# Kernel tuning notes

Hardware: AMD Instinct MI355X
Metric: run time of the kernel (lower is better)

The kernel has to match this reference:

```python
import jax, jax.numpy as jnp
import numpy as np

N_HEAD = 8
HEAD_DIM = 32  # 256 / 8
MASK_VALUE = -10000.0

def setup_inputs() -> dict:
    key = jax.random.key(0)
    k1, k2, k3 = jax.random.split(key, 3)
    B, S, D = 8, 2048, 256
    x = jax.random.normal(k1, (B, S, D), dtype=jnp.float32)
    # kaiming_normal fan_in-based std ~ sqrt(2/fan_in)
    w_qkv = jax.random.normal(k2, (3 * D, D), dtype=jnp.float32) * np.sqrt(2.0 / D)
    b_qkv = jnp.zeros((3 * D,), dtype=jnp.float32)
    w_out = jax.random.normal(k3, (D, D), dtype=jnp.float32) * np.sqrt(2.0 / D)
    b_out = jnp.zeros((D,), dtype=jnp.float32)
    return {"x": x, "w_qkv": w_qkv, "b_qkv": b_qkv, "w_out": w_out, "b_out": b_out}

def reference(x, w_qkv, b_qkv, w_out, b_out):
    B, S, D = x.shape
    qkv = x @ w_qkv.T + b_qkv                      # [B,S,3D]
    q, k, v = jnp.split(qkv, 3, axis=-1)           # each [B,S,D]
    def split_heads(t):
        return t.reshape(B, S, N_HEAD, HEAD_DIM).transpose(0, 2, 1, 3)  # [B,H,S,hd]
    q, k, v = split_heads(q), split_heads(k), split_heads(v)
    scores = jnp.einsum('bhqd,bhkd->bhqk', q, k) / jnp.sqrt(jnp.float32(HEAD_DIM))
    causal = jnp.tril(jnp.ones((S, S), dtype=bool))
    scores = jnp.where(causal[None, None], scores, jnp.float32(MASK_VALUE))
    attn = jax.nn.softmax(scores, axis=-1)          # dropout p=0 (eval)
    out = jnp.einsum('bhqk,bhkd->bhqd', attn, v)    # [B,H,S,hd]
    out = out.transpose(0, 2, 1, 3).reshape(B, S, D)  # merge heads
    out = out @ w_out.T + b_out
    return (out, attn)
```

## Files before the change

### kernel.cpp

```cpp
#include <hip/hip_runtime.h>
#include <cmath>

#define NB 8
#define NS 2048
#define ND 256
#define NH 8
#define HD 32
#define NM (NB*NS)
#define QS_LOG2 (0.17677669529663689f * 1.4426950408889634f)
#define OUT_ATTN ((size_t)NM * ND)

typedef __attribute__((ext_vector_type(8))) short bf16x8;
typedef __attribute__((ext_vector_type(4))) float f32x4;

__device__ __forceinline__ ushort f2b(float f) {
  union { float f; uint32_t u; } v; v.f = f;
  const uint32_t r = (v.u + 0x7FFFu + ((v.u >> 16) & 1u)) >> 16;
  return (ushort)r;
}
__device__ __forceinline__ float b2f(ushort u) {
  union { uint32_t u; float f; } v; v.u = ((uint32_t)u) << 16;
  return v.f;
}

__global__ __launch_bounds__(256) void prep_kernel(
    const float* __restrict__ x, const float* __restrict__ wq,
    const float* __restrict__ wo,
    ushort* __restrict__ xh, ushort* __restrict__ xl,
    ushort* __restrict__ wqh, ushort* __restrict__ wql,
    ushort* __restrict__ woh) {
  const int g = blockIdx.x * 256 + threadIdx.x;
  if (g < 1048576) {
    const float4 v = ((const float4*)x)[g];
    ushort4 h, l;
    h.x = f2b(v.x); l.x = f2b(v.x - b2f(h.x));
    h.y = f2b(v.y); l.y = f2b(v.y - b2f(h.y));
    h.z = f2b(v.z); l.z = f2b(v.z - b2f(h.z));
    h.w = f2b(v.w); l.w = f2b(v.w - b2f(h.w));
    ((ushort4*)xh)[g] = h; ((ushort4*)xl)[g] = l;
  } else if (g < 1048576 + 49152) {
    const int t = g - 1048576;
    const float4 v = ((const float4*)wq)[t];
    ushort4 h, l;
    h.x = f2b(v.x); l.x = f2b(v.x - b2f(h.x));
    h.y = f2b(v.y); l.y = f2b(v.y - b2f(h.y));
    h.z = f2b(v.z); l.z = f2b(v.z - b2f(h.z));
    h.w = f2b(v.w); l.w = f2b(v.w - b2f(h.w));
    ((ushort4*)wqh)[t] = h; ((ushort4*)wql)[t] = l;
  } else if (g < 1048576 + 49152 + 16384) {
    const int t = g - (1048576 + 49152);
    const float4 v = ((const float4*)wo)[t];
    ushort4 h;
    h.x = f2b(v.x); h.y = f2b(v.y); h.z = f2b(v.z); h.w = f2b(v.w);
    ((ushort4*)woh)[t] = h;
  }
}

__global__ __launch_bounds__(256) void qkv_kernel(
    const ushort* __restrict__ xh, const ushort* __restrict__ xl,
    const ushort* __restrict__ wqh, const ushort* __restrict__ wql,
    const float* __restrict__ bias,
    ushort* __restrict__ Qb, ushort* __restrict__ Kb, ushort* __restrict__ Vt) {
  __shared__ ushort Bh[128][40];
  __shared__ ushort Bl[128][40];
  const int m0 = blockIdx.x * 64;
  const int n0 = blockIdx.y * 128;
  const int tid  = threadIdx.x;
  const int w = tid >> 6, lane = tid & 63;
  const int a = lane & 15, qd = lane >> 4;
  const int srow = tid & 127, sop = tid >> 7;
  const f32x4 zero4 = {0.f, 0.f, 0.f, 0.f};
  f32x4 acc[8] = {zero4, zero4, zero4, zero4, zero4, zero4, zero4, zero4};

  const size_t arow = (size_t)(m0 + w*16 + a) * ND;
  const ushort* __restrict__ bsrc = (sop ? wql : wqh) + (size_t)(n0 + srow) * ND;

  for (int ks = 0; ks < 8; ++ks) {
    const int kofs = ks * 32;
    const bf16x8 t0 = *(const bf16x8*)&bsrc[kofs + 0];
    const bf16x8 t1 = *(const bf16x8*)&bsrc[kofs + 8];
    const bf16x8 t2 = *(const bf16x8*)&bsrc[kofs + 16];
    const bf16x8 t3 = *(const bf16x8*)&bsrc[kofs + 24];
    const bf16x8 ah = *(const bf16x8*)&xh[arow + kofs + qd*8];
    const bf16x8 al = *(const bf16x8*)&xl[arow + kofs + qd*8];
    __syncthreads();
    ushort (* __restrict__ Bs)[40] = sop ? Bl : Bh;
    *(bf16x8*)&Bs[srow][0]  = t0;
    *(bf16x8*)&Bs[srow][8]  = t1;
    *(bf16x8*)&Bs[srow][16] = t2;
    *(bf16x8*)&Bs[srow][24] = t3;
    __syncthreads();
#pragma unroll
    for (int nt = 0; nt < 8; ++nt) {
      const bf16x8 bhf = *(const bf16x8*)&Bh[nt*16 + a][qd*8];
      const bf16x8 blf = *(const bf16x8*)&Bl[nt*16 + a][qd*8];
      acc[nt] = __builtin_amdgcn_mfma_f32_16x16x32_bf16(al, bhf, acc[nt], 0, 0, 0);
      acc[nt] = __builtin_amdgcn_mfma_f32_16x16x32_bf16(ah, blf, acc[nt], 0, 0, 0);
      acc[nt] = __builtin_amdgcn_mfma_f32_16x16x32_bf16(ah, bhf, acc[nt], 0, 0, 0);
    }
  }

  const int mbase = m0 + w*16 + qd*4;
  const int bb = mbase >> 11, ss = mbase & 2047;
#pragma unroll
  for (int nt = 0; nt < 8; ++nt) {
    const int n = n0 + nt*16 + a;
    const int which = n >> 8;
    const int h = (n >> 5) & 7, e0 = n & 31;
    const float bz = bias[n];
    if (which < 2) {
      const float scl = (which == 0) ? QS_LOG2 : 1.0f;
      ushort* const dst = ((which == 0) ? Qb : Kb) + (size_t)(bb*NH + h) * NS * HD;
#pragma unroll
      for (int r = 0; r < 4; ++r)
        dst[(size_t)(ss + r) * HD + e0] = f2b((acc[nt][r] + bz) * scl);
    } else {
      ushort4 o;
      o.x = f2b(acc[nt][0] + bz);
      o.y = f2b(acc[nt][1] + bz);
      o.z = f2b(acc[nt][2] + bz);
      o.w = f2b(acc[nt][3] + bz);
      *(ushort4*)&Vt[((size_t)(bb*NH + h)*HD + e0) * NS + ss] = o;
    }
  }
}

__global__ __launch_bounds__(256) void attn_kernel(
    const ushort* __restrict__ Qb, const ushort* __restrict__ Kb,
    const ushort* __restrict__ Vt, float* __restrict__ attn,
    ushort* __restrict__ Om) {
  __shared__ float Ps[2][64][68];
  const int bh = blockIdx.x;
  const int by = blockIdx.y;
  const int qt = (by & 1) ? (by >> 1) : (NS/64 - 1 - (by >> 1));
  const int q0 = qt * 64;
  const int lane = threadIdx.x & 63;
  const int w    = threadIdx.x >> 6;
  const int a    = lane & 15;
  const int qd   = lane >> 4;
  const ushort* __restrict__ Qh = Qb + (size_t)bh * NS * HD;
  const ushort* __restrict__ Kh = Kb + (size_t)bh * NS * HD;
  const ushort* __restrict__ Vh = Vt + (size_t)bh * HD * NS;

  const f32x4 zero4 = {0.f, 0.f, 0.f, 0.f};
  const bf16x8 qf = *(const bf16x8*)&Qh[(size_t)(q0 + w*16 + a) * HD + qd*8];
  float* const attnRow = attn + ((size_t)bh * NS + q0) * NS;

  bf16x8 kf[4], kn[4], vf[4], vp[4];
#pragma unroll
  for (int jt = 0; jt < 4; ++jt)
    kf[jt] = *(const bf16x8*)&Kh[(size_t)(jt*16 + a) * HD + qd*8];

  float l_l[4] = {0.f, 0.f, 0.f, 0.f};
  int zt = qt + 1;
  for (int kt = 0; kt <= qt; ++kt) {
    const bool diag = (kt == qt);
    const int lim = diag ? w : 3;
    if (kt < qt) {
      const int k0n = (kt + 1) * 64;
#pragma unroll
      for (int jt = 0; jt < 4; ++jt)
        kn[jt] = *(const bf16x8*)&Kh[(size_t)(k0n + jt*16 + a) * HD + qd*8];
    }
    if (zt < NS / 64) {
      const int z0 = zt * 64;
#pragma unroll
      for (int i = 0; i < 4; ++i)
        __builtin_nontemporal_store(zero4,
            (f32x4*)&attnRow[(size_t)(w*16 + i*4 + qd) * NS + z0 + a*4]);
      ++zt;
    }
    __builtin_amdgcn_s_setprio(1);
#pragma unroll
    for (int jt = 0; jt < 4; ++jt) {
      if (jt > lim) continue;
      const f32x4 s = __builtin_amdgcn_mfma_f32_16x16x32_bf16(qf, kf[jt], zero4, 0, 0, 0);
      if (diag && jt == w) {
#pragma unroll
        for (int r = 0; r < 4; ++r)
          l_l[r] += (a > qd*4 + r) ? 0.f : exp2f(s[r]);
      } else {
#pragma unroll
        for (int r = 0; r < 4; ++r)
          l_l[r] += exp2f(s[r]);
      }
    }
    __builtin_amdgcn_s_setprio(0);
#pragma unroll
    for (int jt = 0; jt < 4; ++jt) kf[jt] = kn[jt];
  }

#pragma unroll
  for (int jt = 0; jt < 4; ++jt)
    kf[jt] = *(const bf16x8*)&Kh[(size_t)(jt*16 + a) * HD + qd*8];
  vf[0] = *(const bf16x8*)&Vh[(size_t)(a)      * NS + qd*8];
  vf[1] = *(const bf16x8*)&Vh[(size_t)(16 + a) * NS + qd*8];
  vf[2] = *(const bf16x8*)&Vh[(size_t)(a)      * NS + 32 + qd*8];
  vf[3] = *(const bf16x8*)&Vh[(size_t)(16 + a) * NS + 32 + qd*8];

  for (; zt < NS / 64; ++zt) {
    const int z0 = zt * 64;
#pragma unroll
    for (int i = 0; i < 4; ++i)
      __builtin_nontemporal_store(zero4,
          (f32x4*)&attnRow[(size_t)(w*16 + i*4 + qd) * NS + z0 + a*4]);
  }

  float mc[4];
#pragma unroll
  for (int r = 0; r < 4; ++r) {
    float c = l_l[r];
#pragma unroll
    for (int off = 1; off < 16; off <<= 1) c += __shfl_xor(c, off);
    mc[r] = log2f(c);
  }

  f32x4 oc0 = zero4, oc1 = zero4;
  int buf = 0;

  for (int kt = 0; kt <= qt; ++kt) {
    const int k0 = kt * 64;
    const bool diag = (kt == qt);
    const int lim = diag ? w : 3;

    if (kt < qt) {
      const int k0n = k0 + 64;
#pragma unroll
      for (int jt = 0; jt < 4; ++jt)
        kn[jt] = *(const bf16x8*)&Kh[(size_t)(k0n + jt*16 + a) * HD + qd*8];
    }
    if (kt > 0) {
      vf[0] = *(const bf16x8*)&Vh[(size_t)(a)      * NS + k0 + qd*8];
      vf[1] = *(const bf16x8*)&Vh[(size_t)(16 + a) * NS + k0 + qd*8];
      vf[2] = *(const bf16x8*)&Vh[(size_t)(a)      * NS + k0 + 32 + qd*8];
      vf[3] = *(const bf16x8*)&Vh[(size_t)(16 + a) * NS + k0 + 32 + qd*8];
    }

    __builtin_amdgcn_s_setprio(1);
#pragma unroll
    for (int jt = 0; jt < 4; ++jt) {
      if (jt > lim) {
#pragma unroll
        for (int r = 0; r < 4; ++r)
          Ps[buf][w*16 + qd*4 + r][jt*16 + a] = 0.f;
        continue;
      }
      const f32x4 s = __builtin_amdgcn_mfma_f32_16x16x32_bf16(qf, kf[jt], zero4, 0, 0, 0);
      if (diag && jt == w) {
#pragma unroll
        for (int r = 0; r < 4; ++r)
          Ps[buf][w*16 + qd*4 + r][jt*16 + a] =
              (a > qd*4 + r) ? 0.f : exp2f(s[r] - mc[r]);
      } else {
#pragma unroll
        for (int r = 0; r < 4; ++r)
          Ps[buf][w*16 + qd*4 + r][jt*16 + a] = exp2f(s[r] - mc[r]);
      }
    }
    __builtin_amdgcn_s_setprio(0);

#pragma unroll
    for (int i = 0; i < 4; ++i) {
      const int row16 = i*4 + qd;
      const f32x4 pv = *(const f32x4*)&Ps[buf][w*16 + row16][a*4];
      __builtin_nontemporal_store(pv,
          (f32x4*)&attnRow[(size_t)(w*16 + row16) * NS + k0 + a*4]);
    }

    if (kt > 0) {
      __builtin_amdgcn_s_setprio(1);
#pragma unroll
      for (int half = 0; half < 2; ++half) {
        const float4 p0 = *(const float4*)&Ps[buf ^ 1][w*16 + a][half*32 + qd*8];
        const float4 p1 = *(const float4*)&Ps[buf ^ 1][w*16 + a][half*32 + qd*8 + 4];
        bf16x8 pa;
        pa[0] = (short)f2b(p0.x); pa[1] = (short)f2b(p0.y);
        pa[2] = (short)f2b(p0.z); pa[3] = (short)f2b(p0.w);
        pa[4] = (short)f2b(p1.x); pa[5] = (short)f2b(p1.y);
        pa[6] = (short)f2b(p1.z); pa[7] = (short)f2b(p1.w);
        oc0 = __builtin_amdgcn_mfma_f32_16x16x32_bf16(pa, half ? vp[2] : vp[0], oc0, 0, 0, 0);
        oc1 = __builtin_amdgcn_mfma_f32_16x16x32_bf16(pa, half ? vp[3] : vp[1], oc1, 0, 0, 0);
      }
      __builtin_amdgcn_s_setprio(0);
    }

#pragma unroll
    for (int jt = 0; jt < 4; ++jt) { kf[jt] = kn[jt]; vp[jt] = vf[jt]; }
    buf ^= 1;
  }

  {
    __builtin_amdgcn_s_setprio(1);
#pragma unroll
    for (int half = 0; half < 2; ++half) {
      const float4 p0 = *(const float4*)&Ps[buf ^ 1][w*16 + a][half*32 + qd*8];
      const float4 p1 = *(const float4*)&Ps[buf ^ 1][w*16 + a][half*32 + qd*8 + 4];
      bf16x8 pa;
      pa[0] = (short)f2b(p0.x); pa[1] = (short)f2b(p0.y);
      pa[2] = (short)f2b(p0.z); pa[3] = (short)f2b(p0.w);
      pa[4] = (short)f2b(p1.x); pa[5] = (short)f2b(p1.y);
      pa[6] = (short)f2b(p1.z); pa[7] = (short)f2b(p1.w);
      oc0 = __builtin_amdgcn_mfma_f32_16x16x32_bf16(pa, half ? vp[2] : vp[0], oc0, 0, 0, 0);
      oc1 = __builtin_amdgcn_mfma_f32_16x16x32_bf16(pa, half ? vp[3] : vp[1], oc1, 0, 0, 0);
    }
    __builtin_amdgcn_s_setprio(0);
  }

  const int bb = bh >> 3, hh = bh & 7;
#pragma unroll
  for (int r = 0; r < 4; ++r) {
    const size_t om = (size_t)(bb * NS + q0 + w*16 + qd*4 + r) * ND + hh*32;
    Om[om + a]      = f2b(oc0[r]);
    Om[om + 16 + a] = f2b(oc1[r]);
  }
}

__global__ __launch_bounds__(256) void proj_kernel(
    const ushort* __restrict__ Om, const ushort* __restrict__ woh,
    const float* __restrict__ bias, float* __restrict__ out) {
  const int m0 = blockIdx.x * 64;
  const int nb = blockIdx.y * 64;
  const int w = threadIdx.x >> 6, lane = threadIdx.x & 63;
  const int a = lane & 15, qd = lane >> 4;
  const f32x4 zero4 = {0.f, 0.f, 0.f, 0.f};
  f32x4 acc[4] = {zero4, zero4, zero4, zero4};
  const size_t arow = (size_t)(m0 + w*16 + a) * ND;
#pragma unroll
  for (int ks = 0; ks < 8; ++ks) {
    const int kofs = ks * 32 + qd * 8;
    const bf16x8 af = *(const bf16x8*)&Om[arow + kofs];
#pragma unroll
    for (int nt = 0; nt < 4; ++nt) {
      const bf16x8 bfg = *(const bf16x8*)&woh[(size_t)(nb + nt*16 + a) * ND + kofs];
      acc[nt] = __builtin_amdgcn_mfma_f32_16x16x32_bf16(af, bfg, acc[nt], 0, 0, 0);
    }
  }
#pragma unroll
  for (int nt = 0; nt < 4; ++nt) {
    const int n = nb + nt*16 + a;
    const float bz = bias[n];
#pragma unroll
    for (int r = 0; r < 4; ++r)
      out[(size_t)(m0 + w*16 + qd*4 + r) * ND + n] = acc[nt][r] + bz;
  }
}

extern "C" void kernel_launch(void* const* d_in, const int* in_sizes, int n_in,
                              void* d_out, int out_size, void* d_ws, size_t ws_size,
                              hipStream_t stream) {
  const float* x     = (const float*)d_in[0];
  const float* w_qkv = (const float*)d_in[1];
  const float* b_qkv = (const float*)d_in[2];
  const float* w_out = (const float*)d_in[3];
  const float* b_out = (const float*)d_in[4];
  float* out  = (float*)d_out;
  float* attn = out + OUT_ATTN;

  ushort* u = (ushort*)d_ws;
  const size_t SZH = (size_t)NB * NH * NS * HD;
  ushort* Qb  = u;  u += SZH;
  ushort* Kb  = u;  u += SZH;
  ushort* Vt  = u;  u += SZH;
  ushort* Om  = u;  u += SZH;
  ushort* xh  = u;  u += SZH;
  ushort* xl  = u;  u += SZH;
  ushort* wqh = u;  u += (size_t)768 * ND;
  ushort* wql = u;  u += (size_t)768 * ND;
  ushort* woh = u;  u += (size_t)ND * ND;

  prep_kernel<<<4352, 256, 0, stream>>>(x, w_qkv, w_out, xh, xl, wqh, wql, woh);
  qkv_kernel<<<dim3(NM / 64, 768 / 128), 256, 0, stream>>>(xh, xl, wqh, wql, b_qkv, Qb, Kb, Vt);
  attn_kernel<<<dim3(NB * NH, NS / 64), 256, 0, stream>>>(Qb, Kb, Vt, attn, Om);
  proj_kernel<<<dim3(NM / 64, ND / 64), 256, 0, stream>>>(Om, woh, b_out, out);
}
```

Measured before the change: 307.9 us.

## Pair high and low causal query tiles per block for load balance

Each attention block now handles two query tiles, one from the top and one from the bottom of the causal triangle (j and NS/64-1-j), so every block does roughly the same amount of work. The grid is halved. Zero-fill stores for one tile are interleaved with the row-sum pass of the other, which is meant to hide store traffic behind compute. In exchange there are half as many blocks to fill the GPU, and register pressure rises from holding two Q fragments and two sets of softmax statistics.

```diff
diff --git a/kernel.cpp b/kernel.cpp
--- a/kernel.cpp
+++ b/kernel.cpp
@@ -131,9 +131,10 @@
     ushort* __restrict__ Om) {
   __shared__ float Ps[2][64][68];
   const int bh = blockIdx.x;
-  const int by = blockIdx.y;
-  const int qt = (by & 1) ? (by >> 1) : (NS/64 - 1 - (by >> 1));
-  const int q0 = qt * 64;
+  const int j  = blockIdx.y;
+  const int qtH = NS/64 - 1 - j;
+  const int qtL = j;
+  const int q0H = qtH * 64, q0L = qtL * 64;
   const int lane = threadIdx.x & 63;
   const int w    = threadIdx.x >> 6;
   const int a    = lane & 15;
@@ -143,46 +144,49 @@
   const ushort* __restrict__ Vh = Vt + (size_t)bh * HD * NS;
 
   const f32x4 zero4 = {0.f, 0.f, 0.f, 0.f};
-  const bf16x8 qf = *(const bf16x8*)&Qh[(size_t)(q0 + w*16 + a) * HD + qd*8];
-  float* const attnRow = attn + ((size_t)bh * NS + q0) * NS;
+  const bf16x8 qfH = *(const bf16x8*)&Qh[(size_t)(q0H + w*16 + a) * HD + qd*8];
+  const bf16x8 qfL = *(const bf16x8*)&Qh[(size_t)(q0L + w*16 + a) * HD + qd*8];
+  float* const rowH = attn + ((size_t)bh * NS + q0H) * NS;
+  float* const rowL = attn + ((size_t)bh * NS + q0L) * NS;
 
   bf16x8 kf[4], kn[4], vf[4], vp[4];
+
 #pragma unroll
   for (int jt = 0; jt < 4; ++jt)
     kf[jt] = *(const bf16x8*)&Kh[(size_t)(jt*16 + a) * HD + qd*8];
 
-  float l_l[4] = {0.f, 0.f, 0.f, 0.f};
-  int zt = qt + 1;
-  for (int kt = 0; kt <= qt; ++kt) {
-    const bool diag = (kt == qt);
+  float llH[4] = {0.f, 0.f, 0.f, 0.f};
+  int ztL = qtL + 1;
+  for (int kt = 0; kt <= qtH; ++kt) {
+    const bool diag = (kt == qtH);
     const int lim = diag ? w : 3;
-    if (kt < qt) {
+    if (kt < qtH) {
       const int k0n = (kt + 1) * 64;
 #pragma unroll
       for (int jt = 0; jt < 4; ++jt)
         kn[jt] = *(const bf16x8*)&Kh[(size_t)(k0n + jt*16 + a) * HD + qd*8];
     }
-    if (zt < NS / 64) {
-      const int z0 = zt * 64;
+    if (ztL < NS / 64) {
+      const int z0 = ztL * 64;
 #pragma unroll
       for (int i = 0; i < 4; ++i)
         __builtin_nontemporal_store(zero4,
-            (f32x4*)&attnRow[(size_t)(w*16 + i*4 + qd) * NS + z0 + a*4]);
-      ++zt;
+            (f32x4*)&rowL[(size_t)(w*16 + i*4 + qd) * NS + z0 + a*4]);
+      ++ztL;
     }
     __builtin_amdgcn_s_setprio(1);
 #pragma unroll
     for (int jt = 0; jt < 4; ++jt) {
       if (jt > lim) continue;
-      const f32x4 s = __builtin_amdgcn_mfma_f32_16x16x32_bf16(qf, kf[jt], zero4, 0, 0, 0);
+      const f32x4 s = __builtin_amdgcn_mfma_f32_16x16x32_bf16(qfH, kf[jt], zero4, 0, 0, 0);
       if (diag && jt == w) {
 #pragma unroll
         for (int r = 0; r < 4; ++r)
-          l_l[r] += (a > qd*4 + r) ? 0.f : exp2f(s[r]);
+          llH[r] += (a > qd*4 + r) ? 0.f : exp2f(s[r]);
       } else {
 #pragma unroll
         for (int r = 0; r < 4; ++r)
-          l_l[r] += exp2f(s[r]);
+          llH[r] += exp2f(s[r]);
       }
     }
     __builtin_amdgcn_s_setprio(0);
@@ -193,103 +197,165 @@
 #pragma unroll
   for (int jt = 0; jt < 4; ++jt)
     kf[jt] = *(const bf16x8*)&Kh[(size_t)(jt*16 + a) * HD + qd*8];
-  vf[0] = *(const bf16x8*)&Vh[(size_t)(a)      * NS + qd*8];
-  vf[1] = *(const bf16x8*)&Vh[(size_t)(16 + a) * NS + qd*8];
-  vf[2] = *(const bf16x8*)&Vh[(size_t)(a)      * NS + 32 + qd*8];
-  vf[3] = *(const bf16x8*)&Vh[(size_t)(16 + a) * NS + 32 + qd*8];
-
-  for (; zt < NS / 64; ++zt) {
-    const int z0 = zt * 64;
+
+  float llL[4] = {0.f, 0.f, 0.f, 0.f};
+  int ztH = qtH + 1;
+  for (int kt = 0; kt <= qtL; ++kt) {
+    const bool diag = (kt == qtL);
+    const int lim = diag ? w : 3;
+    if (kt < qtL) {
+      const int k0n = (kt + 1) * 64;
+#pragma unroll
+      for (int jt = 0; jt < 4; ++jt)
+        kn[jt] = *(const bf16x8*)&Kh[(size_t)(k0n + jt*16 + a) * HD + qd*8];
+    }
+    if (ztH < NS / 64) {
+      const int z0 = ztH * 64;
+#pragma unroll
+      for (int i = 0; i < 4; ++i)
+        __builtin_nontemporal_store(zero4,
+            (f32x4*)&rowH[(size_t)(w*16 + i*4 + qd) * NS + z0 + a*4]);
+      ++ztH;
+    }
+    __builtin_amdgcn_s_setprio(1);
+#pragma unroll
+    for (int jt = 0; jt < 4; ++jt) {
+      if (jt > lim) continue;
+      const f32x4 s = __builtin_amdgcn_mfma_f32_16x16x32_bf16(qfL, kf[jt], zero4, 0, 0, 0);
+      if (diag && jt == w) {
+#pragma unroll
+        for (int r = 0; r < 4; ++r)
+          llL[r] += (a > qd*4 + r) ? 0.f : exp2f(s[r]);
+      } else {
+#pragma unroll
+        for (int r = 0; r < 4; ++r)
+          llL[r] += exp2f(s[r]);
+      }
+    }
+    __builtin_amdgcn_s_setprio(0);
+#pragma unroll
+    for (int jt = 0; jt < 4; ++jt) kf[jt] = kn[jt];
+  }
+
+  for (; ztL < NS / 64; ++ztL) {
+    const int z0 = ztL * 64;
 #pragma unroll
     for (int i = 0; i < 4; ++i)
       __builtin_nontemporal_store(zero4,
-          (f32x4*)&attnRow[(size_t)(w*16 + i*4 + qd) * NS + z0 + a*4]);
-  }
-
-  float mc[4];
+          (f32x4*)&rowL[(size_t)(w*16 + i*4 + qd) * NS + z0 + a*4]);
+  }
+  for (; ztH < NS / 64; ++ztH) {
+    const int z0 = ztH * 64;
+#pragma unroll
+    for (int i = 0; i < 4; ++i)
+      __builtin_nontemporal_store(zero4,
+          (f32x4*)&rowH[(size_t)(w*16 + i*4 + qd) * NS + z0 + a*4]);
+  }
+
+  float mcH[4], mcL[4];
 #pragma unroll
   for (int r = 0; r < 4; ++r) {
-    float c = l_l[r];
+    float c = llH[r];
 #pragma unroll
     for (int off = 1; off < 16; off <<= 1) c += __shfl_xor(c, off);
-    mc[r] = log2f(c);
-  }
-
-  f32x4 oc0 = zero4, oc1 = zero4;
-  int buf = 0;
-
-  for (int kt = 0; kt <= qt; ++kt) {
-    const int k0 = kt * 64;
-    const bool diag = (kt == qt);
-    const int lim = diag ? w : 3;
-
-    if (kt < qt) {
-      const int k0n = k0 + 64;
-#pragma unroll
-      for (int jt = 0; jt < 4; ++jt)
-        kn[jt] = *(const bf16x8*)&Kh[(size_t)(k0n + jt*16 + a) * HD + qd*8];
-    }
-    if (kt > 0) {
-      vf[0] = *(const bf16x8*)&Vh[(size_t)(a)      * NS + k0 + qd*8];
-      vf[1] = *(const bf16x8*)&Vh[(size_t)(16 + a) * NS + k0 + qd*8];
-      vf[2] = *(const bf16x8*)&Vh[(size_t)(a)      * NS + k0 + 32 + qd*8];
-      vf[3] = *(const bf16x8*)&Vh[(size_t)(16 + a) * NS + k0 + 32 + qd*8];
-    }
-
-    __builtin_amdgcn_s_setprio(1);
-#pragma unroll
-    for (int jt = 0; jt < 4; ++jt) {
-      if (jt > lim) {
-#pragma unroll
-        for (int r = 0; r < 4; ++r)
-          Ps[buf][w*16 + qd*4 + r][jt*16 + a] = 0.f;
-        continue;
-      }
-      const f32x4 s = __builtin_amdgcn_mfma_f32_16x16x32_bf16(qf, kf[jt], zero4, 0, 0, 0);
-      if (diag && jt == w) {
-#pragma unroll
-        for (int r = 0; r < 4; ++r)
-          Ps[buf][w*16 + qd*4 + r][jt*16 + a] =
-              (a > qd*4 + r) ? 0.f : exp2f(s[r] - mc[r]);
-      } else {
-#pragma unroll
-        for (int r = 0; r < 4; ++r)
-          Ps[buf][w*16 + qd*4 + r][jt*16 + a] = exp2f(s[r] - mc[r]);
-      }
-    }
-    __builtin_amdgcn_s_setprio(0);
-
-#pragma unroll
-    for (int i = 0; i < 4; ++i) {
-      const int row16 = i*4 + qd;
-      const f32x4 pv = *(const f32x4*)&Ps[buf][w*16 + row16][a*4];
-      __builtin_nontemporal_store(pv,
-          (f32x4*)&attnRow[(size_t)(w*16 + row16) * NS + k0 + a*4]);
-    }
-
-    if (kt > 0) {
+    mcH[r] = log2f(c);
+    float d = llL[r];
+#pragma unroll
+    for (int off = 1; off < 16; off <<= 1) d += __shfl_xor(d, off);
+    mcL[r] = log2f(d);
+  }
+
+  const int bb = bh >> 3, hh = bh & 7;
+
+  for (int pass = 0; pass < 2; ++pass) {
+    const int qt = pass ? qtL : qtH;
+    const int q0 = pass ? q0L : q0H;
+    const bf16x8 qf = pass ? qfL : qfH;
+    const float* mc = pass ? mcL : mcH;
+    float* const attnRow = pass ? rowL : rowH;
+
+#pragma unroll
+    for (int jt = 0; jt < 4; ++jt)
+      kf[jt] = *(const bf16x8*)&Kh[(size_t)(jt*16 + a) * HD + qd*8];
+    vf[0] = *(const bf16x8*)&Vh[(size_t)(a)      * NS + qd*8];
+    vf[1] = *(const bf16x8*)&Vh[(size_t)(16 + a) * NS + qd*8];
+    vf[2] = *(const bf16x8*)&Vh[(size_t)(a)      * NS + 32 + qd*8];
+    vf[3] = *(const bf16x8*)&Vh[(size_t)(16 + a) * NS + 32 + qd*8];
+
+    f32x4 oc0 = zero4, oc1 = zero4;
+    int buf = 0;
+
+    for (int kt = 0; kt <= qt; ++kt) {
+      const int k0 = kt * 64;
+      const bool diag = (kt == qt);
+      const int lim = diag ? w : 3;
+
+      if (kt < qt) {
+        const int k0n = k0 + 64;
+#pragma unroll
+        for (int jt = 0; jt < 4; ++jt)
+          kn[jt] = *(const bf16x8*)&Kh[(size_t)(k0n + jt*16 + a) * HD + qd*8];
+      }
+      if (kt > 0) {
+        vf[0] = *(const bf16x8*)&Vh[(size_t)(a)      * NS + k0 + qd*8];
+        vf[1] = *(const bf16x8*)&Vh[(size_t)(16 + a) * NS + k0 + qd*8];
+        vf[2] = *(const bf16x8*)&Vh[(size_t)(a)      * NS + k0 + 32 + qd*8];
+        vf[3] = *(const bf16x8*)&Vh[(size_t)(16 + a) * NS + k0 + 32 + qd*8];
+      }
+
       __builtin_amdgcn_s_setprio(1);
 #pragma unroll
-      for (int half = 0; half < 2; ++half) {
-        const float4 p0 = *(const float4*)&Ps[buf ^ 1][w*16 + a][half*32 + qd*8];
-        const float4 p1 = *(const float4*)&Ps[buf ^ 1][w*16 + a][half*32 + qd*8 + 4];
-        bf16x8 pa;
-        pa[0] = (short)f2b(p0.x); pa[1] = (short)f2b(p0.y);
-        pa[2] = (short)f2b(p0.z); pa[3] = (short)f2b(p0.w);
-        pa[4] = (short)f2b(p1.x); pa[5] = (short)f2b(p1.y);
-        pa[6] = (short)f2b(p1.z); pa[7] = (short)f2b(p1.w);
-        oc0 = __builtin_amdgcn_mfma_f32_16x16x32_bf16(pa, half ? vp[2] : vp[0], oc0, 0, 0, 0);
-        oc1 = __builtin_amdgcn_mfma_f32_16x16x32_bf16(pa, half ? vp[3] : vp[1], oc1, 0, 0, 0);
+      for (int jt = 0; jt < 4; ++jt) {
+        if (jt > lim) {
+#pragma unroll
+          for (int r = 0; r < 4; ++r)
+            Ps[buf][w*16 + qd*4 + r][jt*16 + a] = 0.f;
+          continue;
+        }
+        const f32x4 s = __builtin_amdgcn_mfma_f32_16x16x32_bf16(qf, kf[jt], zero4, 0, 0, 0);
+        if (diag && jt == w) {
+#pragma unroll
+          for (int r = 0; r < 4; ++r)
+            Ps[buf][w*16 + qd*4 + r][jt*16 + a] =
+                (a > qd*4 + r) ? 0.f : exp2f(s[r] - mc[r]);
+        } else {
+#pragma unroll
+          for (int r = 0; r < 4; ++r)
+            Ps[buf][w*16 + qd*4 + r][jt*16 + a] = exp2f(s[r] - mc[r]);
+        }
       }
       __builtin_amdgcn_s_setprio(0);
-    }
-
-#pragma unroll
-    for (int jt = 0; jt < 4; ++jt) { kf[jt] = kn[jt]; vp[jt] = vf[jt]; }
-    buf ^= 1;
-  }
-
-  {
+
+#pragma unroll
+      for (int i = 0; i < 4; ++i) {
+        const int row16 = i*4 + qd;
+        const f32x4 pv = *(const f32x4*)&Ps[buf][w*16 + row16][a*4];
+        __builtin_nontemporal_store(pv,
+            (f32x4*)&attnRow[(size_t)(w*16 + row16) * NS + k0 + a*4]);
+      }
+
+      if (kt > 0) {
+        __builtin_amdgcn_s_setprio(1);
+#pragma unroll
+        for (int half = 0; half < 2; ++half) {
+          const float4 p0 = *(const float4*)&Ps[buf ^ 1][w*16 + a][half*32 + qd*8];
+          const float4 p1 = *(const float4*)&Ps[buf ^ 1][w*16 + a][half*32 + qd*8 + 4];
+          bf16x8 pa;
+          pa[0] = (short)f2b(p0.x); pa[1] = (short)f2b(p0.y);
+          pa[2] = (short)f2b(p0.z); pa[3] = (short)f2b(p0.w);
+          pa[4] = (short)f2b(p1.x); pa[5] = (short)f2b(p1.y);
+          pa[6] = (short)f2b(p1.z); pa[7] = (short)f2b(p1.w);
+          oc0 = __builtin_amdgcn_mfma_f32_16x16x32_bf16(pa, half ? vp[2] : vp[0], oc0, 0, 0, 0);
+          oc1 = __builtin_amdgcn_mfma_f32_16x16x32_bf16(pa, half ? vp[3] : vp[1], oc1, 0, 0, 0);
+        }
+        __builtin_amdgcn_s_setprio(0);
+      }
+
+#pragma unroll
+      for (int jt = 0; jt < 4; ++jt) { kf[jt] = kn[jt]; vp[jt] = vf[jt]; }
+      buf ^= 1;
+    }
+
     __builtin_amdgcn_s_setprio(1);
 #pragma unroll
     for (int half = 0; half < 2; ++half) {
@@ -304,14 +370,13 @@
       oc1 = __builtin_amdgcn_mfma_f32_16x16x32_bf16(pa, half ? vp[3] : vp[1], oc1, 0, 0, 0);
     }
     __builtin_amdgcn_s_setprio(0);
-  }
-
-  const int bb = bh >> 3, hh = bh & 7;
-#pragma unroll
-  for (int r = 0; r < 4; ++r) {
-    const size_t om = (size_t)(bb * NS + q0 + w*16 + qd*4 + r) * ND + hh*32;
-    Om[om + a]      = f2b(oc0[r]);
-    Om[om + 16 + a] = f2b(oc1[r]);
+
+#pragma unroll
+    for (int r = 0; r < 4; ++r) {
+      const size_t om = (size_t)(bb * NS + q0 + w*16 + qd*4 + r) * ND + hh*32;
+      Om[om + a]      = f2b(oc0[r]);
+      Om[om + 16 + a] = f2b(oc1[r]);
+    }
   }
 }
 
@@ -370,6 +435,6 @@
 
   prep_kernel<<<4352, 256, 0, stream>>>(x, w_qkv, w_out, xh, xl, wqh, wql, woh);
   qkv_kernel<<<dim3(NM / 64, 768 / 128), 256, 0, stream>>>(xh, xl, wqh, wql, b_qkv, Qb, Kb, Vt);
-  attn_kernel<<<dim3(NB * NH, NS / 64), 256, 0, stream>>>(Qb, Kb, Vt, attn, Om);
+  attn_kernel<<<dim3(NB * NH, NS / 128), 256, 0, stream>>>(Qb, Kb, Vt, attn, Om);
   proj_kernel<<<dim3(NM / 64, ND / 64), 256, 0, stream>>>(Om, woh, b_out, out);
 }
```

Result: slower. 319.8 us (+3.8%).
